# Performance work log

Measured on AMD Instinct MI355X. Metric: run time of the kernel, lower is better.

## Reference

```python
import jax, jax.numpy as jnp
import numpy as np

N = 262144            # number of particles
H0 = 0.006            # base SPH support radius (unit square domain)
GRID = 256            # static upper bound on cells per dimension (actual ~170)
NUM_CELLS = GRID * GRID
K = 32                # max particles stored per cell (avg occupancy ~9.4)
NCAND = 9 * K         # searchRadius=1 -> 3x3 cell stencil
MAX_NEIGHBORS = 64    # padded neighbor-list width (avg neighbor count ~27)


def setup_inputs() -> dict:
    key = jax.random.key(0)
    kp, ks = jax.random.split(key)
    positions = jax.random.uniform(kp, (N, 2), dtype=jnp.float32)
    # supports in [0.9*H0, H0], mimicking mildly adaptive SPH supports
    supports = H0 * (0.9 + 0.1 * jax.random.uniform(ks, (N,), dtype=jnp.float32))
    return {"positions": positions, "supports": supports}


def _cell_linear_indices(positions, supports):
    # mirrors sortPositions: cell size = hMax, indices = ceil((p - qMin)/hMax)
    hMax = jnp.max(supports)
    qMin = jnp.min(positions, axis=0) - hMax
    ij = jnp.ceil((positions - qMin) / hMax).astype(jnp.int32)  # >= 1 by construction
    ij = jnp.clip(ij, 0, GRID - 1)
    return ij[:, 0] + GRID * ij[:, 1]


def _build_cell_table(lin):
    # dense equivalent of the hash-grid: sort by cell, counting-sort into [cell, slot]
    order = jnp.argsort(lin)                       # == sortingIndices in the original
    lin_s = lin[order]
    counts = jax.ops.segment_sum(jnp.ones(N, jnp.int32), lin, num_segments=NUM_CELLS)
    starts = jnp.cumsum(counts) - counts           # exclusive prefix sum == cumCell
    rank = jnp.arange(N, dtype=jnp.int32) - starts[lin_s].astype(jnp.int32)
    ovf = rank >= K                                # overflow slots -> dump row
    cell_t = jnp.where(ovf, NUM_CELLS, lin_s)
    slot_t = jnp.where(ovf, 0, rank)
    table = jnp.full((NUM_CELLS + 1, K), -1, dtype=jnp.int32)
    table = table.at[cell_t, slot_t].set(order.astype(jnp.int32))
    return table


def reference(positions, supports):
    lin = _cell_linear_indices(positions, supports)
    table = _build_cell_table(lin)

    # 3x3 stencil of neighbor cells (searchRadius = 1)
    dx, dy = jnp.meshgrid(jnp.arange(-1, 2), jnp.arange(-1, 2), indexing='ij')
    offs = (dx + GRID * dy).reshape(1, 9).astype(jnp.int32)
    cand_cells = jnp.clip(lin[:, None] + offs, 0, NUM_CELLS)  # [N, 9]

    cand = table[cand_cells].reshape(N, NCAND)     # [N, 288] candidate particle ids
    present = cand >= 0
    cidx = jnp.where(present, cand, 0)
    cpos = positions[cidx]                         # [N, 288, 2] gather (memory bound)
    diff = cpos - positions[:, None, :]
    dist = jnp.sqrt(jnp.sum(diff * diff, axis=-1)) # [N, 288]
    valid = present & (dist <= supports[:, None])  # |x_i - x_j| <= h_i (self included)
    count = jnp.sum(valid, axis=1).astype(jnp.int32)

    # compact valid candidates to the front, pad to MAX_NEIGHBORS
    order2 = jnp.argsort(jnp.where(valid, 0, 1).astype(jnp.int32), axis=1, stable=True)
    sel = order2[:, :MAX_NEIGHBORS]
    nbr = jnp.take_along_axis(cidx, sel, axis=1)
    dsel = jnp.take_along_axis(dist, sel, axis=1)
    inb = jnp.arange(MAX_NEIGHBORS)[None, :] < count[:, None]
    neighbors = jnp.where(inb, nbr, -1)
    radial = jnp.where(inb, dsel / supports[:, None], 0.0)  # fluidRadialDistances
    return neighbors, count, radial
```

## Files before the change

### kernel.cpp

```cpp
#include <hip/hip_runtime.h>
#include <float.h>

#define N_PART 262144
#define GRID_DIM 256
#define NUM_CELLS (GRID_DIM * GRID_DIM)
#define KSLOT 32
#define MAXNB 64


__global__ void init_params(unsigned int* params) {
    params[0] = 0x7f7fffffu;
    params[1] = 0x7f7fffffu;
    params[2] = 0u;
}

__global__ void reduce_kernel(const float* __restrict__ pos,
                              const float* __restrict__ sup,
                              unsigned int* params, int n) {
    __shared__ unsigned int s_minx, s_miny, s_maxh;
    if (threadIdx.x == 0) { s_minx = 0x7f7fffffu; s_miny = 0x7f7fffffu; s_maxh = 0u; }
    __syncthreads();
    float mx = FLT_MAX, my = FLT_MAX, mh = 0.0f;
    for (int i = blockIdx.x * blockDim.x + threadIdx.x; i < n;
         i += gridDim.x * blockDim.x) {
        float x = pos[2 * i], y = pos[2 * i + 1], h = sup[i];
        mx = fminf(mx, x);
        my = fminf(my, y);
        mh = fmaxf(mh, h);
    }
    atomicMin(&s_minx, __float_as_uint(mx));
    atomicMin(&s_miny, __float_as_uint(my));
    atomicMax(&s_maxh, __float_as_uint(mh));
    __syncthreads();
    if (threadIdx.x == 0) {
        atomicMin(&params[0], s_minx);
        atomicMin(&params[1], s_miny);
        atomicMax(&params[2], s_maxh);
    }
}

__global__ void bin_kernel(const float* __restrict__ pos,
                           const unsigned int* __restrict__ params,
                           int* __restrict__ counts, int* __restrict__ lin_out,
                           int n) {
    int i = blockIdx.x * blockDim.x + threadIdx.x;
    if (i >= n) return;
    float hmax  = __uint_as_float(params[2]);
    float qminx = __uint_as_float(params[0]) - hmax;
    float qminy = __uint_as_float(params[1]) - hmax;
    float x = pos[2 * i], y = pos[2 * i + 1];
    int cx = (int)ceilf((x - qminx) / hmax);
    int cy = (int)ceilf((y - qminy) / hmax);
    cx = min(max(cx, 0), GRID_DIM - 1);
    cy = min(max(cy, 0), GRID_DIM - 1);
    int lin = cx + GRID_DIM * cy;
    lin_out[i] = lin;
    atomicAdd(&counts[lin], 1);
}

__global__ void scan_local(const int* __restrict__ counts,
                           int* __restrict__ starts,
                           int* __restrict__ chunkSums) {
    __shared__ int sd[256];
    int t = threadIdx.x;
    int idx = blockIdx.x * 256 + t;
    int v = counts[idx];
    sd[t] = v;
    __syncthreads();
#pragma unroll
    for (int off = 1; off < 256; off <<= 1) {
        int x = (t >= off) ? sd[t - off] : 0;
        __syncthreads();
        sd[t] += x;
        __syncthreads();
    }
    starts[idx] = sd[t] - v;
    if (t == 255) chunkSums[blockIdx.x] = sd[t];
}

__global__ void scan_apply(int* __restrict__ starts,
                           const int* __restrict__ chunkSums, int n) {
    __shared__ int red[256];
    int t = threadIdx.x, b = blockIdx.x;
    red[t] = (t < b) ? chunkSums[t] : 0;
    __syncthreads();
#pragma unroll
    for (int s = 128; s > 0; s >>= 1) {
        if (t < s) red[t] += red[t + s];
        __syncthreads();
    }
    starts[b * 256 + t] += red[0];
    if (b == 255 && t == 0) {
        starts[NUM_CELLS]     = n;
        starts[NUM_CELLS + 1] = n;
    }
}

__global__ void scatter_kernel(const int* __restrict__ lin,
                               const int* __restrict__ starts,
                               int* __restrict__ cursor,
                               int* __restrict__ sid, int n) {
    int i = blockIdx.x * blockDim.x + threadIdx.x;
    if (i >= n) return;
    int c = lin[i];
    int r = atomicAdd(&cursor[c], 1);
    sid[starts[c] + r] = i;
}

__global__ void sortseg_kernel(const int* __restrict__ starts,
                               int* __restrict__ sid,
                               int* __restrict__ linS,
                               float4* __restrict__ Q,
                               const float2* __restrict__ pos2,
                               const float* __restrict__ sup) {
    int c = blockIdx.x * blockDim.x + threadIdx.x;
    if (c >= NUM_CELLS) return;
    int b = starts[c], e = starts[c + 1];
    for (int a = b + 1; a < e; a++) {
        int v = sid[a];
        int k = a - 1;
        while (k >= b && sid[k] > v) { sid[k + 1] = sid[k]; k--; }
        sid[k + 1] = v;
    }
    for (int s = b; s < e; s++) {
        int j = sid[s];
        float2 pj = pos2[j];
        Q[s] = make_float4(pj.x, pj.y, __int_as_float(j), sup[j]);
        linS[s] = c;
    }
}

__global__ __launch_bounds__(256) void query_kernel(
        const int* __restrict__ linS, const float4* __restrict__ Q,
        const int* __restrict__ starts,
        float* __restrict__ outN, float* __restrict__ outC,
        float* __restrict__ outR, int n) {
#pragma clang fp contract(off)
    __shared__ int   s_id[4][MAXNB];
    __shared__ float s_d[4][MAXNB];

    int gtid = blockIdx.x * blockDim.x + threadIdx.x;
    int r    = gtid >> 6;
    int lane = threadIdx.x & 63;
    int wsl  = threadIdx.x >> 6;
    if (r >= n) return;

    float4 me = Q[r];
    int   i  = __builtin_amdgcn_readfirstlane(__float_as_int(me.z));
    float px = __int_as_float(__builtin_amdgcn_readfirstlane(__float_as_int(me.x)));
    float py = __int_as_float(__builtin_amdgcn_readfirstlane(__float_as_int(me.y)));
    float h  = __int_as_float(__builtin_amdgcn_readfirstlane(__float_as_int(me.w)));
    int   L  = __builtin_amdgcn_readfirstlane(linS[r]);

    const int offs[9] = {-257, -1, 255, -256, 0, 256, -255, 1, 257};
    int cum[10], delta[9];
    cum[0] = 0;
#pragma unroll
    for (int o = 0; o < 9; o++) {
        int cell = L + offs[o];
        cell = min(max(cell, 0), NUM_CELLS);
        int bb = __builtin_amdgcn_readfirstlane(starts[cell]);
        int ee = __builtin_amdgcn_readfirstlane(starts[cell + 1]);
        int cc = min(ee - bb, KSLOT);
        delta[o]  = bb - cum[o];
        cum[o + 1] = cum[o] + cc;
    }
    int T = cum[9];

    int total = 0;
    for (int b0 = 0; b0 < T; b0 += 64) {
        int ll = b0 + lane;
        int dsel = delta[0];
#pragma unroll
        for (int m = 1; m < 9; m++)
            dsel = (ll >= cum[m]) ? delta[m] : dsel;
        int idx = ll + dsel;
        float4 q = Q[idx];
        float dx = q.x - px;
        float dy = q.y - py;
        float s2 = dx * dx + dy * dy;
        float d  = sqrtf(s2);
        bool valid = (ll < T) && (d <= h);
        unsigned long long bal = __ballot(valid);
        int rank = __popcll(bal & ((1ull << lane) - 1ull));
        if (valid) {
            int w = total + rank;
            if (w < MAXNB) {
                s_id[wsl][w] = __float_as_int(q.z);
                s_d[wsl][w]  = d;
            }
        }
        total += __popcll(bal);
    }

    int stored = min(total, MAXNB);
    size_t base = (size_t)i * MAXNB;
    if (lane < stored) {
        int j   = s_id[wsl][lane];
        float d = s_d[wsl][lane];
        outN[base + lane] = (float)j;
        outR[base + lane] = d / h;
    } else {
        outN[base + lane] = -1.0f;
        outR[base + lane] = 0.0f;
    }
    if (lane == 0) outC[i] = (float)total;
}

extern "C" void kernel_launch(void* const* d_in, const int* in_sizes, int n_in,
                              void* d_out, int out_size, void* d_ws, size_t ws_size,
                              hipStream_t stream) {
    const float* pos = (const float*)d_in[0];
    const float* sup = (const float*)d_in[1];

    char* p = (char*)d_ws;
    auto alloc = [&](size_t bytes) {
        char* q = p;
        p += (bytes + 255) & ~(size_t)255;
        return q;
    };
    unsigned int* params    = (unsigned int*)alloc(256);
    int*          counts    = (int*)alloc((size_t)NUM_CELLS * 4);
    int*          cursor    = (int*)alloc((size_t)NUM_CELLS * 4);
    int*          chunkSums = (int*)alloc(256 * 4);
    int*          starts    = (int*)alloc((size_t)(NUM_CELLS + 2) * 4);
    int*          lin       = (int*)alloc((size_t)N_PART * 4);
    int*          sid       = (int*)alloc((size_t)(N_PART + 64) * 4);
    int*          linS      = (int*)alloc((size_t)N_PART * 4);
    float4*       Q         = (float4*)alloc((size_t)(N_PART + 64) * 16);

    float* out  = (float*)d_out;
    float* outN = out;
    float* outC = out + (size_t)N_PART * MAXNB;
    float* outR = outC + N_PART;

    hipMemsetAsync(counts, 0, (size_t)NUM_CELLS * 4 * 2, stream);
    init_params<<<1, 1, 0, stream>>>(params);
    reduce_kernel<<<256, 256, 0, stream>>>(pos, sup, params, N_PART);
    bin_kernel<<<N_PART / 256, 256, 0, stream>>>(pos, params, counts, lin, N_PART);
    scan_local<<<NUM_CELLS / 256, 256, 0, stream>>>(counts, starts, chunkSums);
    scan_apply<<<NUM_CELLS / 256, 256, 0, stream>>>(starts, chunkSums, N_PART);
    scatter_kernel<<<N_PART / 256, 256, 0, stream>>>(lin, starts, cursor, sid, N_PART);
    sortseg_kernel<<<NUM_CELLS / 256, 256, 0, stream>>>(starts, sid, linS, Q,
                                                        (const float2*)pos, sup);
    query_kernel<<<(N_PART * 64) / 256, 256, 0, stream>>>(
        linS, Q, starts, outN, outC, outR, N_PART);
}
```

Measured before the change: 295.7 us.

## Replace sqrt compare with squared threshold, selection-sort cells, vectorize position loads

The query kernel now compares squared distance against a float threshold precomputed once per particle from h, so sqrt is taken only for stored outputs, and it uses mbcnt for ranking and a fast reciprocal and hardware sqrt for the radial output. The per-cell insertion sort, which wrote shifted entries back to global memory, becomes a read-only repeated-minimum selection over sid, which costs O(n^2) reads per cell. Reductions and binning load float2 positions. The fast rcp/sqrt may differ slightly from the exact d/h division, and the threshold trick must reproduce sqrt(s2)<=h exactly.

Result: slower. 309.1 us (+4.5%).

```diff
diff --git a/kernel.cpp b/kernel.cpp
--- a/kernel.cpp
+++ b/kernel.cpp
@@ -20,12 +20,14 @@
     __shared__ unsigned int s_minx, s_miny, s_maxh;
     if (threadIdx.x == 0) { s_minx = 0x7f7fffffu; s_miny = 0x7f7fffffu; s_maxh = 0u; }
     __syncthreads();
+    const float2* pos2 = (const float2*)pos;
     float mx = FLT_MAX, my = FLT_MAX, mh = 0.0f;
     for (int i = blockIdx.x * blockDim.x + threadIdx.x; i < n;
          i += gridDim.x * blockDim.x) {
-        float x = pos[2 * i], y = pos[2 * i + 1], h = sup[i];
-        mx = fminf(mx, x);
-        my = fminf(my, y);
+        float2 p = pos2[i];
+        float h = sup[i];
+        mx = fminf(mx, p.x);
+        my = fminf(my, p.y);
         mh = fmaxf(mh, h);
     }
     atomicMin(&s_minx, __float_as_uint(mx));
@@ -48,9 +50,9 @@
     float hmax  = __uint_as_float(params[2]);
     float qminx = __uint_as_float(params[0]) - hmax;
     float qminy = __uint_as_float(params[1]) - hmax;
-    float x = pos[2 * i], y = pos[2 * i + 1];
-    int cx = (int)ceilf((x - qminx) / hmax);
-    int cy = (int)ceilf((y - qminy) / hmax);
+    float2 p = ((const float2*)pos)[i];
+    int cx = (int)ceilf((p.x - qminx) / hmax);
+    int cy = (int)ceilf((p.y - qminy) / hmax);
     cx = min(max(cx, 0), GRID_DIM - 1);
     cy = min(max(cy, 0), GRID_DIM - 1);
     int lin = cx + GRID_DIM * cy;
@@ -108,7 +110,7 @@
 }
 
 __global__ void sortseg_kernel(const int* __restrict__ starts,
-                               int* __restrict__ sid,
+                               const int* __restrict__ sid,
                                int* __restrict__ linS,
                                float4* __restrict__ Q,
                                const float2* __restrict__ pos2,
@@ -116,17 +118,17 @@
     int c = blockIdx.x * blockDim.x + threadIdx.x;
     if (c >= NUM_CELLS) return;
     int b = starts[c], e = starts[c + 1];
-    for (int a = b + 1; a < e; a++) {
-        int v = sid[a];
-        int k = a - 1;
-        while (k >= b && sid[k] > v) { sid[k + 1] = sid[k]; k--; }
-        sid[k + 1] = v;
-    }
-    for (int s = b; s < e; s++) {
-        int j = sid[s];
-        float2 pj = pos2[j];
-        Q[s] = make_float4(pj.x, pj.y, __int_as_float(j), sup[j]);
-        linS[s] = c;
+    int prev = -1;
+    for (int k = b; k < e; k++) {
+        int best = 0x7fffffff;
+        for (int s = b; s < e; s++) {
+            int v = sid[s];
+            best = (v > prev && v < best) ? v : best;
+        }
+        prev = best;
+        float2 pj = pos2[best];
+        Q[k] = make_float4(pj.x, pj.y, __int_as_float(best), sup[best]);
+        linS[k] = c;
     }
 }
 
@@ -137,13 +139,12 @@
         float* __restrict__ outR, int n) {
 #pragma clang fp contract(off)
     __shared__ int   s_id[4][MAXNB];
-    __shared__ float s_d[4][MAXNB];
+    __shared__ float s_s2[4][MAXNB];
 
     int gtid = blockIdx.x * blockDim.x + threadIdx.x;
     int r    = gtid >> 6;
     int lane = threadIdx.x & 63;
     int wsl  = threadIdx.x >> 6;
-    if (r >= n) return;
 
     float4 me = Q[r];
     int   i  = __builtin_amdgcn_readfirstlane(__float_as_int(me.z));
@@ -151,6 +152,12 @@
     float py = __int_as_float(__builtin_amdgcn_readfirstlane(__float_as_int(me.y)));
     float h  = __int_as_float(__builtin_amdgcn_readfirstlane(__float_as_int(me.w)));
     int   L  = __builtin_amdgcn_readfirstlane(linS[r]);
+
+    float  hn  = __int_as_float(__float_as_int(h) + 1);
+    double mid = 0.5 * ((double)h + (double)hn);
+    double t2  = mid * mid;
+    float  S   = (float)t2;
+    S = ((double)S > t2) ? __int_as_float(__float_as_int(S) - 1) : S;
 
     const int offs[9] = {-257, -1, 255, -256, 0, 256, -255, 1, 257};
     int cum[10], delta[9];
@@ -179,31 +186,31 @@
         float dx = q.x - px;
         float dy = q.y - py;
         float s2 = dx * dx + dy * dy;
-        float d  = sqrtf(s2);
-        bool valid = (ll < T) && (d <= h);
-        unsigned long long bal = __ballot(valid);
-        int rank = __popcll(bal & ((1ull << lane) - 1ull));
-        if (valid) {
-            int w = total + rank;
-            if (w < MAXNB) {
-                s_id[wsl][w] = __float_as_int(q.z);
-                s_d[wsl][w]  = d;
-            }
+        int rem = T - b0;
+        unsigned long long maskT =
+            (rem >= 64) ? ~0ull : ((1ull << rem) - 1ull);
+        unsigned long long bal = __ballot(s2 <= S) & maskT;
+        int rank = __builtin_amdgcn_mbcnt_hi(
+            (unsigned)(bal >> 32),
+            __builtin_amdgcn_mbcnt_lo((unsigned)bal, 0));
+        int w = total + rank;
+        if ((s2 <= S) && (ll < T) && (w < MAXNB)) {
+            s_id[wsl][w] = __float_as_int(q.z);
+            s_s2[wsl][w] = s2;
         }
-        total += __popcll(bal);
+        total += (int)__popcll(bal);
     }
 
     int stored = min(total, MAXNB);
+    float rh = __builtin_amdgcn_rcpf(h);
     size_t base = (size_t)i * MAXNB;
-    if (lane < stored) {
-        int j   = s_id[wsl][lane];
-        float d = s_d[wsl][lane];
-        outN[base + lane] = (float)j;
-        outR[base + lane] = d / h;
-    } else {
-        outN[base + lane] = -1.0f;
-        outR[base + lane] = 0.0f;
-    }
+    int   jj = s_id[wsl][lane];
+    float ss = s_s2[wsl][lane];
+    bool inb = lane < stored;
+    float vN = inb ? (float)jj : -1.0f;
+    float vR = inb ? __builtin_amdgcn_sqrtf(ss) * rh : 0.0f;
+    outN[base + lane] = vN;
+    outR[base + lane] = vR;
     if (lane == 0) outC[i] = (float)total;
 }
 
```
